# Optimization experiments

Hardware: AMD Instinct MI355X
Metric: run time of the kernel (lower is better)

Reference implementation:

```python
import jax, jax.numpy as jnp
import numpy as np

B, H, O, M = 8192, 1024, 1024, 4

def setup_inputs() -> dict:
    key = jax.random.key(0)
    ks = jax.random.split(key, 8)
    state = jax.random.normal(ks[0], (B, H), dtype=jnp.float32)
    spectral_entropy = jax.random.uniform(ks[1], (B, 1), dtype=jnp.float32)
    curvature = jax.random.normal(ks[2], (B, 1), dtype=jnp.float32)
    # learned params
    modulation_basis = jax.random.normal(ks[3], (M, H, O), dtype=jnp.float32)
    gate_w = jax.random.normal(ks[4], (1, M), dtype=jnp.float32) / jnp.sqrt(1.0)
    gate_b = jax.random.normal(ks[5], (M,), dtype=jnp.float32) * 0.01
    prj_w = jax.random.normal(ks[6], (H, O), dtype=jnp.float32) / jnp.sqrt(H)
    prj_b = jax.random.normal(ks[7], (O,), dtype=jnp.float32) * 0.01
    return {"state": state, "spectral_entropy": spectral_entropy, "curvature": curvature,
            "modulation_basis": modulation_basis, "gate_w": gate_w, "gate_b": gate_b,
            "prj_w": prj_w, "prj_b": prj_b}

def reference(state, spectral_entropy, curvature, modulation_basis, gate_w, gate_b, prj_w, prj_b):
    # softmax gate over modes: [B, M]
    mod_weights = jax.nn.softmax(spectral_entropy @ gate_w + gate_b, axis=-1)
    # Algebraically fused form of einsum('bm,mho->bho') then einsum('bh,bho->bo'):
    # compute per-mode matvec results [B, M, O] (small), then mode-weighted sum.
    mode_out = jnp.einsum('bh,mho->bmo', state, modulation_basis)
    mischief_output = jnp.einsum('bm,bmo->bo', mod_weights, mode_out)
    base_output = state @ prj_w + prj_b
    mix = jax.nn.sigmoid(curvature)  # [B, 1]
    return (1.0 - mix) * base_output + mix * mischief_output
```

## Files before the change

### kernel.cpp

```cpp
#include <hip/hip_runtime.h>
#include <stdint.h>

typedef __attribute__((ext_vector_type(4))) float  float4v;
typedef __attribute__((ext_vector_type(8))) __bf16 bf16x8;
typedef __attribute__((ext_vector_type(8))) unsigned short ushort8;

#define B_DIM 8192
#define H_DIM 1024
#define O_DIM 1024

static __device__ __forceinline__ unsigned short f32_to_bf16(float f) {
  union { float f; unsigned int u; } v; v.f = f;
  unsigned int u = v.u;
  unsigned int r = u + 0x7FFFu + ((u >> 16) & 1u);
  return (unsigned short)(r >> 16);
}

__global__ void prep_inputs(const float* __restrict__ state,
                            const float* __restrict__ basis,
                            const float* __restrict__ prjw,
                            unsigned short* __restrict__ Abf,
                            unsigned short* __restrict__ Wt) {
  __shared__ __align__(16) unsigned short t[64 * 72];
  int bb = blockIdx.x;
  int tid = threadIdx.x;
  if (bb < 1280) {
    int m = bb >> 8, panel = bb & 255;
    int o0 = (panel & 15) * 64, h0 = (panel >> 4) * 64;
    const float* src = (m < 4) ? (basis + (size_t)m * H_DIM * O_DIM) : prjw;
    int r  = tid >> 4;
    int c4 = (tid & 15) * 4;
#pragma unroll
    for (int p = 0; p < 4; ++p) {
      int h = r + p * 16;
      float4v v = *(const float4v*)(src + (size_t)(h0 + h) * O_DIM + o0 + c4);
      t[(c4 + 0) * 72 + h] = f32_to_bf16(v.x);
      t[(c4 + 1) * 72 + h] = f32_to_bf16(v.y);
      t[(c4 + 2) * 72 + h] = f32_to_bf16(v.z);
      t[(c4 + 3) * 72 + h] = f32_to_bf16(v.w);
    }
    __syncthreads();
#pragma unroll
    for (int i = 0; i < 2; ++i) {
      int C = i * 256 + tid;
      int o = C >> 3, cc = C & 7;
      ushort8 val = *(const ushort8*)(t + o * 72 + cc * 8);
      *(ushort8*)(Wt + ((size_t)m * O_DIM + o0 + o) * H_DIM + h0 + cc * 8) = val;
    }
  } else {
    int i = (bb - 1280) * 256 + tid;
    float4v v0 = ((const float4v*)state)[i * 2];
    float4v v1 = ((const float4v*)state)[i * 2 + 1];
    ushort8 o;
    o[0] = f32_to_bf16(v0.x); o[1] = f32_to_bf16(v0.y);
    o[2] = f32_to_bf16(v0.z); o[3] = f32_to_bf16(v0.w);
    o[4] = f32_to_bf16(v1.x); o[5] = f32_to_bf16(v1.y);
    o[6] = f32_to_bf16(v1.z); o[7] = f32_to_bf16(v1.w);
    ((ushort8*)Abf)[i] = o;
  }
}

__global__ __launch_bounds__(256, 2)
void gemm_fused(const unsigned short* __restrict__ A,
                const unsigned short* __restrict__ Wt,
                const float* __restrict__ se, const float* __restrict__ curv,
                const float* __restrict__ gw, const float* __restrict__ gb,
                const float* __restrict__ prjb,
                float* __restrict__ out) {
  __shared__ __align__(16) unsigned char smem[59904];
  float* scf = (float*)(smem + 57344);

  const int tid  = threadIdx.x;
  const int lane = tid & 63;
  const int wave = tid >> 6;
  const int row0 = blockIdx.x * 128;
  const int col0 = blockIdx.y * 64;
  const int wrow = (wave >> 1) * 64;
  const int wcol = (wave & 1) * 32;
  const int q  = lane >> 4;
  const int ln = lane & 15;

  if (tid < 128) {
    int b = row0 + tid;
    float s = se[b];
    float l0 = fmaf(s, gw[0], gb[0]);
    float l1 = fmaf(s, gw[1], gb[1]);
    float l2 = fmaf(s, gw[2], gb[2]);
    float l3 = fmaf(s, gw[3], gb[3]);
    float mx = fmaxf(fmaxf(l0, l1), fmaxf(l2, l3));
    float e0 = __expf(l0 - mx), e1 = __expf(l1 - mx);
    float e2 = __expf(l2 - mx), e3 = __expf(l3 - mx);
    float mix = 1.0f / (1.0f + __expf(-curv[b]));
    float inv = mix / (e0 + e1 + e2 + e3);
    scf[0 * 128 + tid] = e0 * inv;
    scf[1 * 128 + tid] = e1 * inv;
    scf[2 * 128 + tid] = e2 * inv;
    scf[3 * 128 + tid] = e3 * inv;
    scf[4 * 128 + tid] = 1.0f - mix;
  }

  const unsigned short* gA[2];
  unsigned int ldsA[2];
#pragma unroll
  for (int j = 0; j < 2; ++j) {
    int C = (wave * 2 + j) * 64 + lane;
    int row = C >> 2, pos = C & 3;
    int g = pos ^ ((row >> 1) & 3);
    gA[j] = A + (size_t)(row0 + row) * H_DIM + g * 8;
    ldsA[j] = (wave * 2 + j) * 1024;
  }
  const unsigned short* gB[5];
  unsigned int ldsBbase = 8192 + wave * 1024;
  {
    int C = wave * 64 + lane;
    int row = C >> 2, pos = C & 3;
    int g = pos ^ ((row >> 1) & 3);
#pragma unroll
    for (int m = 0; m < 5; ++m)
      gB[m] = Wt + (size_t)m * O_DIM * H_DIM + (size_t)(col0 + row) * H_DIM + g * 8;
  }

  float4v acc[5][4][2];
#pragma unroll
  for (int m = 0; m < 5; ++m)
#pragma unroll
    for (int i = 0; i < 4; ++i)
#pragma unroll
      for (int j = 0; j < 2; ++j)
        acc[m][i][j] = (float4v){0.f, 0.f, 0.f, 0.f};

#define ISSUE_STAGE(s)                                                          \
  do {                                                                          \
    const int _buf = (s) & 1;                                                   \
    const int _k = (s) * 32;                                                    \
    unsigned char* _base = smem + _buf * 28672;                                 \
    _Pragma("unroll")                                                           \
    for (int _j = 0; _j < 2; ++_j)                                              \
      __builtin_amdgcn_global_load_lds(                                         \
          (const __attribute__((address_space(1))) void*)(gA[_j] + _k),         \
          (__attribute__((address_space(3))) void*)(_base + ldsA[_j]), 16, 0, 0);\
    _Pragma("unroll")                                                           \
    for (int _m = 0; _m < 5; ++_m)                                              \
      __builtin_amdgcn_global_load_lds(                                         \
          (const __attribute__((address_space(1))) void*)(gB[_m] + _k),         \
          (__attribute__((address_space(3))) void*)(_base + ldsBbase + _m * 4096),\
          16, 0, 0);                                                            \
  } while (0)

#define COMPUTE_STAGE(s)                                                        \
  do {                                                                          \
    const unsigned short* _sA = (const unsigned short*)(smem + ((s) & 1) * 28672);\
    const unsigned short* _sB = _sA + 4096;                                     \
    bf16x8 _af[4];                                                              \
    _Pragma("unroll")                                                           \
    for (int _t = 0; _t < 4; ++_t) {                                            \
      int _ra = wrow + _t * 16 + ln;                                            \
      int _ps = q ^ ((_ra >> 1) & 3);                                           \
      _af[_t] = *(const bf16x8*)(_sA + _ra * 32 + _ps * 8);                     \
    }                                                                           \
    _Pragma("unroll")                                                           \
    for (int _m = 0; _m < 5; ++_m) {                                            \
      bf16x8 _b0, _b1;                                                          \
      {                                                                         \
        int _rb = wcol + ln;                                                    \
        int _p0 = q ^ ((_rb >> 1) & 3);                                         \
        _b0 = *(const bf16x8*)(_sB + _m * 2048 + _rb * 32 + _p0 * 8);           \
        int _r1 = wcol + 16 + ln;                                               \
        int _p1 = q ^ ((_r1 >> 1) & 3);                                         \
        _b1 = *(const bf16x8*)(_sB + _m * 2048 + _r1 * 32 + _p1 * 8);           \
      }                                                                         \
      _Pragma("unroll")                                                         \
      for (int _ti = 0; _ti < 4; ++_ti) {                                       \
        acc[_m][_ti][0] = __builtin_amdgcn_mfma_f32_16x16x32_bf16(              \
            _af[_ti], _b0, acc[_m][_ti][0], 0, 0, 0);                           \
        acc[_m][_ti][1] = __builtin_amdgcn_mfma_f32_16x16x32_bf16(              \
            _af[_ti], _b1, acc[_m][_ti][1], 0, 0, 0);                           \
      }                                                                         \
    }                                                                           \
  } while (0)

  ISSUE_STAGE(0);
  __syncthreads();
#pragma unroll 2
  for (int s = 0; s < 31; ++s) {
    ISSUE_STAGE(s + 1);
    COMPUTE_STAGE(s);
    __syncthreads();
  }
  COMPUTE_STAGE(31);

  __syncthreads();
  float* fbuf = (float*)smem;
#pragma unroll
  for (int ti = 0; ti < 4; ++ti) {
    int rl = wrow + ti * 16 + q * 4;
#pragma unroll
    for (int tj = 0; tj < 2; ++tj) {
      int cc = wcol + tj * 16 + ln;
#pragma unroll
      for (int r = 0; r < 4; ++r) {
        float v = 0.f;
#pragma unroll
        for (int m = 0; m < 5; ++m)
          v += scf[m * 128 + rl + r] * acc[m][ti][tj][r];
        fbuf[(rl + r) * 68 + cc] = v;
      }
    }
  }
  __syncthreads();
#pragma unroll
  for (int i = 0; i < 8; ++i) {
    int L = i * 256 + tid;
    int row = L >> 4, c4 = L & 15;
    float4v v = *(const float4v*)(fbuf + row * 68 + c4 * 4);
    float cb = scf[4 * 128 + row];
    float4v pb = *(const float4v*)(prjb + col0 + c4 * 4);
    v += cb * pb;
    *(float4v*)(out + (size_t)(row0 + row) * O_DIM + col0 + c4 * 4) = v;
  }
#undef ISSUE_STAGE
#undef COMPUTE_STAGE
}

extern "C" void kernel_launch(void* const* d_in, const int* in_sizes, int n_in,
                              void* d_out, int out_size, void* d_ws, size_t ws_size,
                              hipStream_t stream) {
  const float* state = (const float*)d_in[0];
  const float* se    = (const float*)d_in[1];
  const float* curv  = (const float*)d_in[2];
  const float* basis = (const float*)d_in[3];
  const float* gw    = (const float*)d_in[4];
  const float* gb    = (const float*)d_in[5];
  const float* prjw  = (const float*)d_in[6];
  const float* prjb  = (const float*)d_in[7];
  float* out = (float*)d_out;

  char* ws = (char*)d_ws;
  unsigned short* Abf = (unsigned short*)ws;
  unsigned short* Wt  = (unsigned short*)(ws + (size_t)16 * 1024 * 1024);

  prep_inputs<<<5376, 256, 0, stream>>>(state, basis, prjw, Abf, Wt);
  dim3 gg(B_DIM / 128, O_DIM / 64);
  gemm_fused<<<gg, 256, 0, stream>>>(Abf, Wt, se, curv, gw, gb, prjb, out);
}
```

Before: 183.7 us.

## Fuse state bf16 cast into GEMM and load operands directly from global memory

Drops the separate cast of state to bf16 in the prep kernel; the GEMM now reads fp32 state rows directly and packs them to bf16 in registers. It also removes the LDS double-buffered global_load_lds pipeline and has each wave load its A and B fragments straight from global memory into registers, shrinking shared memory to the epilogue buffer. This avoids a 16 MB bf16 intermediate write/read and the LDS staging barriers. The cost is that every wave re-reads A and B fragments from global or cache with no LDS sharing or software prefetch, and the A traffic doubles because it is fp32.

```diff
diff --git a/kernel.cpp b/kernel.cpp
--- a/kernel.cpp
+++ b/kernel.cpp
@@ -8,6 +8,7 @@
 #define B_DIM 8192
 #define H_DIM 1024
 #define O_DIM 1024
+#define MSTRIDE (O_DIM * H_DIM)
 
 static __device__ __forceinline__ unsigned short f32_to_bf16(float f) {
   union { float f; unsigned int u; } v; v.f = f;
@@ -16,59 +17,54 @@
   return (unsigned short)(r >> 16);
 }
 
-__global__ void prep_inputs(const float* __restrict__ state,
-                            const float* __restrict__ basis,
-                            const float* __restrict__ prjw,
-                            unsigned short* __restrict__ Abf,
-                            unsigned short* __restrict__ Wt) {
+static __device__ __forceinline__ bf16x8 pack8(float4v a, float4v b) {
+  union { ushort8 u; bf16x8 h; } c;
+  c.u[0] = f32_to_bf16(a.x); c.u[1] = f32_to_bf16(a.y);
+  c.u[2] = f32_to_bf16(a.z); c.u[3] = f32_to_bf16(a.w);
+  c.u[4] = f32_to_bf16(b.x); c.u[5] = f32_to_bf16(b.y);
+  c.u[6] = f32_to_bf16(b.z); c.u[7] = f32_to_bf16(b.w);
+  return c.h;
+}
+
+__global__ void transpose_cast(const float* __restrict__ basis, const float* __restrict__ prjw,
+                               unsigned short* __restrict__ Wt) {
   __shared__ __align__(16) unsigned short t[64 * 72];
   int bb = blockIdx.x;
+  int m = bb >> 8, panel = bb & 255;
+  int o0 = (panel & 15) * 64, h0 = (panel >> 4) * 64;
+  const float* src = (m < 4) ? (basis + (size_t)m * H_DIM * O_DIM) : prjw;
   int tid = threadIdx.x;
-  if (bb < 1280) {
-    int m = bb >> 8, panel = bb & 255;
-    int o0 = (panel & 15) * 64, h0 = (panel >> 4) * 64;
-    const float* src = (m < 4) ? (basis + (size_t)m * H_DIM * O_DIM) : prjw;
-    int r  = tid >> 4;
-    int c4 = (tid & 15) * 4;
+  int r  = tid >> 4;
+  int c4 = (tid & 15) * 4;
 #pragma unroll
-    for (int p = 0; p < 4; ++p) {
-      int h = r + p * 16;
-      float4v v = *(const float4v*)(src + (size_t)(h0 + h) * O_DIM + o0 + c4);
-      t[(c4 + 0) * 72 + h] = f32_to_bf16(v.x);
-      t[(c4 + 1) * 72 + h] = f32_to_bf16(v.y);
-      t[(c4 + 2) * 72 + h] = f32_to_bf16(v.z);
-      t[(c4 + 3) * 72 + h] = f32_to_bf16(v.w);
-    }
-    __syncthreads();
+  for (int p = 0; p < 4; ++p) {
+    int h = r + p * 16;
+    float4v v = *(const float4v*)(src + (size_t)(h0 + h) * O_DIM + o0 + c4);
+    t[(c4 + 0) * 72 + h] = f32_to_bf16(v.x);
+    t[(c4 + 1) * 72 + h] = f32_to_bf16(v.y);
+    t[(c4 + 2) * 72 + h] = f32_to_bf16(v.z);
+    t[(c4 + 3) * 72 + h] = f32_to_bf16(v.w);
+  }
+  __syncthreads();
 #pragma unroll
-    for (int i = 0; i < 2; ++i) {
-      int C = i * 256 + tid;
-      int o = C >> 3, cc = C & 7;
-      ushort8 val = *(const ushort8*)(t + o * 72 + cc * 8);
-      *(ushort8*)(Wt + ((size_t)m * O_DIM + o0 + o) * H_DIM + h0 + cc * 8) = val;
-    }
-  } else {
-    int i = (bb - 1280) * 256 + tid;
-    float4v v0 = ((const float4v*)state)[i * 2];
-    float4v v1 = ((const float4v*)state)[i * 2 + 1];
-    ushort8 o;
-    o[0] = f32_to_bf16(v0.x); o[1] = f32_to_bf16(v0.y);
-    o[2] = f32_to_bf16(v0.z); o[3] = f32_to_bf16(v0.w);
-    o[4] = f32_to_bf16(v1.x); o[5] = f32_to_bf16(v1.y);
-    o[6] = f32_to_bf16(v1.z); o[7] = f32_to_bf16(v1.w);
-    ((ushort8*)Abf)[i] = o;
+  for (int i = 0; i < 2; ++i) {
+    int C = i * 256 + tid;
+    int o = C >> 3, cc = C & 7;
+    ushort8 val = *(const ushort8*)(t + o * 72 + cc * 8);
+    *(ushort8*)(Wt + ((size_t)m * O_DIM + o0 + o) * H_DIM + h0 + cc * 8) = val;
   }
 }
 
 __global__ __launch_bounds__(256, 2)
-void gemm_fused(const unsigned short* __restrict__ A,
+void gemm_fused(const float* __restrict__ state,
                 const unsigned short* __restrict__ Wt,
                 const float* __restrict__ se, const float* __restrict__ curv,
                 const float* __restrict__ gw, const float* __restrict__ gb,
                 const float* __restrict__ prjb,
                 float* __restrict__ out) {
-  __shared__ __align__(16) unsigned char smem[59904];
-  float* scf = (float*)(smem + 57344);
+  __shared__ __align__(16) unsigned char smem[37376];
+  float* fbuf = (float*)smem;
+  float* scf  = (float*)(smem + 34816);
 
   const int tid  = threadIdx.x;
   const int lane = tid & 63;
@@ -99,26 +95,12 @@
     scf[4 * 128 + tid] = 1.0f - mix;
   }
 
-  const unsigned short* gA[2];
-  unsigned int ldsA[2];
+  const float* aptr[4];
 #pragma unroll
-  for (int j = 0; j < 2; ++j) {
-    int C = (wave * 2 + j) * 64 + lane;
-    int row = C >> 2, pos = C & 3;
-    int g = pos ^ ((row >> 1) & 3);
-    gA[j] = A + (size_t)(row0 + row) * H_DIM + g * 8;
-    ldsA[j] = (wave * 2 + j) * 1024;
-  }
-  const unsigned short* gB[5];
-  unsigned int ldsBbase = 8192 + wave * 1024;
-  {
-    int C = wave * 64 + lane;
-    int row = C >> 2, pos = C & 3;
-    int g = pos ^ ((row >> 1) & 3);
-#pragma unroll
-    for (int m = 0; m < 5; ++m)
-      gB[m] = Wt + (size_t)m * O_DIM * H_DIM + (size_t)(col0 + row) * H_DIM + g * 8;
-  }
+  for (int t = 0; t < 4; ++t)
+    aptr[t] = state + (size_t)(row0 + wrow + t * 16 + ln) * H_DIM + q * 8;
+  const unsigned short* bptr0 = Wt + (size_t)(col0 + wcol + ln)      * H_DIM + q * 8;
+  const unsigned short* bptr1 = Wt + (size_t)(col0 + wcol + 16 + ln) * H_DIM + q * 8;
 
   float4v acc[5][4][2];
 #pragma unroll
@@ -129,68 +111,29 @@
       for (int j = 0; j < 2; ++j)
         acc[m][i][j] = (float4v){0.f, 0.f, 0.f, 0.f};
 
-#define ISSUE_STAGE(s)                                                          \
-  do {                                                                          \
-    const int _buf = (s) & 1;                                                   \
-    const int _k = (s) * 32;                                                    \
-    unsigned char* _base = smem + _buf * 28672;                                 \
-    _Pragma("unroll")                                                           \
-    for (int _j = 0; _j < 2; ++_j)                                              \
-      __builtin_amdgcn_global_load_lds(                                         \
-          (const __attribute__((address_space(1))) void*)(gA[_j] + _k),         \
-          (__attribute__((address_space(3))) void*)(_base + ldsA[_j]), 16, 0, 0);\
-    _Pragma("unroll")                                                           \
-    for (int _m = 0; _m < 5; ++_m)                                              \
-      __builtin_amdgcn_global_load_lds(                                         \
-          (const __attribute__((address_space(1))) void*)(gB[_m] + _k),         \
-          (__attribute__((address_space(3))) void*)(_base + ldsBbase + _m * 4096),\
-          16, 0, 0);                                                            \
-  } while (0)
-
-#define COMPUTE_STAGE(s)                                                        \
-  do {                                                                          \
-    const unsigned short* _sA = (const unsigned short*)(smem + ((s) & 1) * 28672);\
-    const unsigned short* _sB = _sA + 4096;                                     \
-    bf16x8 _af[4];                                                              \
-    _Pragma("unroll")                                                           \
-    for (int _t = 0; _t < 4; ++_t) {                                            \
-      int _ra = wrow + _t * 16 + ln;                                            \
-      int _ps = q ^ ((_ra >> 1) & 3);                                           \
-      _af[_t] = *(const bf16x8*)(_sA + _ra * 32 + _ps * 8);                     \
-    }                                                                           \
-    _Pragma("unroll")                                                           \
-    for (int _m = 0; _m < 5; ++_m) {                                            \
-      bf16x8 _b0, _b1;                                                          \
-      {                                                                         \
-        int _rb = wcol + ln;                                                    \
-        int _p0 = q ^ ((_rb >> 1) & 3);                                         \
-        _b0 = *(const bf16x8*)(_sB + _m * 2048 + _rb * 32 + _p0 * 8);           \
-        int _r1 = wcol + 16 + ln;                                               \
-        int _p1 = q ^ ((_r1 >> 1) & 3);                                         \
-        _b1 = *(const bf16x8*)(_sB + _m * 2048 + _r1 * 32 + _p1 * 8);           \
-      }                                                                         \
-      _Pragma("unroll")                                                         \
-      for (int _ti = 0; _ti < 4; ++_ti) {                                       \
-        acc[_m][_ti][0] = __builtin_amdgcn_mfma_f32_16x16x32_bf16(              \
-            _af[_ti], _b0, acc[_m][_ti][0], 0, 0, 0);                           \
-        acc[_m][_ti][1] = __builtin_amdgcn_mfma_f32_16x16x32_bf16(              \
-            _af[_ti], _b1, acc[_m][_ti][1], 0, 0, 0);                           \
-      }                                                                         \
-    }                                                                           \
-  } while (0)
-
-  ISSUE_STAGE(0);
-  __syncthreads();
 #pragma unroll 2
-  for (int s = 0; s < 31; ++s) {
-    ISSUE_STAGE(s + 1);
-    COMPUTE_STAGE(s);
-    __syncthreads();
+  for (int s = 0; s < 32; ++s) {
+    const int k = s * 32;
+    bf16x8 af[4];
+#pragma unroll
+    for (int t = 0; t < 4; ++t) {
+      float4v u0 = *(const float4v*)(aptr[t] + k);
+      float4v u1 = *(const float4v*)(aptr[t] + k + 4);
+      af[t] = pack8(u0, u1);
+    }
+#pragma unroll
+    for (int m = 0; m < 5; ++m) {
+      bf16x8 b0 = *(const bf16x8*)(bptr0 + (size_t)m * MSTRIDE + k);
+      bf16x8 b1 = *(const bf16x8*)(bptr1 + (size_t)m * MSTRIDE + k);
+#pragma unroll
+      for (int ti = 0; ti < 4; ++ti) {
+        acc[m][ti][0] = __builtin_amdgcn_mfma_f32_16x16x32_bf16(af[ti], b0, acc[m][ti][0], 0, 0, 0);
+        acc[m][ti][1] = __builtin_amdgcn_mfma_f32_16x16x32_bf16(af[ti], b1, acc[m][ti][1], 0, 0, 0);
+      }
+    }
   }
-  COMPUTE_STAGE(31);
 
   __syncthreads();
-  float* fbuf = (float*)smem;
 #pragma unroll
   for (int ti = 0; ti < 4; ++ti) {
     int rl = wrow + ti * 16 + q * 4;
@@ -218,8 +161,6 @@
     v += cb * pb;
     *(float4v*)(out + (size_t)(row0 + row) * O_DIM + col0 + c4 * 4) = v;
   }
-#undef ISSUE_STAGE
-#undef COMPUTE_STAGE
 }
 
 extern "C" void kernel_launch(void* const* d_in, const int* in_sizes, int n_in,
@@ -235,11 +176,9 @@
   const float* prjb  = (const float*)d_in[7];
   float* out = (float*)d_out;
 
-  char* ws = (char*)d_ws;
-  unsigned short* Abf = (unsigned short*)ws;
-  unsigned short* Wt  = (unsigned short*)(ws + (size_t)16 * 1024 * 1024);
+  unsigned short* Wt = (unsigned short*)d_ws;
 
-  prep_inputs<<<5376, 256, 0, stream>>>(state, basis, prjw, Abf, Wt);
+  transpose_cast<<<1280, 256, 0, stream>>>(basis, prjw, Wt);
   dim3 gg(B_DIM / 128, O_DIM / 64);
-  gemm_fused<<<gg, 256, 0, stream>>>(Abf, Wt, se, curv, gw, gb, prjb, out);
+  gemm_fused<<<gg, 256, 0, stream>>>(state, Wt, se, curv, gw, gb, prjb, out);
 }
```

New measurement: 378.9 us. 106% more time.

## Apply per-row mode coefficients each k-step to shrink accumulators to one set

Applied to the files above, without the earlier changes.

Instead of keeping five separate MFMA accumulator sets (one per mode plus base) and combining them with per-row coefficients at the end, each MFMA now starts from zero and its result is scaled by per-row coefficients held in registers and added into a single accumulator set. This cuts accumulator registers roughly fivefold, which could raise occupancy or stop spills. In exchange it adds a vector FMA per MFMA, so the accumulation chain runs through VALU ops and MFMA outputs cannot be chained, which may stall the matrix pipe. Rounding also shifts slightly because the scaling happens per k-step.

```diff
diff --git a/kernel.cpp b/kernel.cpp
--- a/kernel.cpp
+++ b/kernel.cpp
@@ -120,20 +120,10 @@
       gB[m] = Wt + (size_t)m * O_DIM * H_DIM + (size_t)(col0 + row) * H_DIM + g * 8;
   }
 
-  float4v acc[5][4][2];
-#pragma unroll
-  for (int m = 0; m < 5; ++m)
-#pragma unroll
-    for (int i = 0; i < 4; ++i)
-#pragma unroll
-      for (int j = 0; j < 2; ++j)
-        acc[m][i][j] = (float4v){0.f, 0.f, 0.f, 0.f};
-
 #define ISSUE_STAGE(s)                                                          \
   do {                                                                          \
-    const int _buf = (s) & 1;                                                   \
+    unsigned char* _base = smem + ((s) & 1) * 28672;                            \
     const int _k = (s) * 32;                                                    \
-    unsigned char* _base = smem + _buf * 28672;                                 \
     _Pragma("unroll")                                                           \
     for (int _j = 0; _j < 2; ++_j)                                              \
       __builtin_amdgcn_global_load_lds(                                         \
@@ -147,49 +137,59 @@
           16, 0, 0);                                                            \
   } while (0)
 
-#define COMPUTE_STAGE(s)                                                        \
-  do {                                                                          \
-    const unsigned short* _sA = (const unsigned short*)(smem + ((s) & 1) * 28672);\
-    const unsigned short* _sB = _sA + 4096;                                     \
-    bf16x8 _af[4];                                                              \
-    _Pragma("unroll")                                                           \
-    for (int _t = 0; _t < 4; ++_t) {                                            \
-      int _ra = wrow + _t * 16 + ln;                                            \
-      int _ps = q ^ ((_ra >> 1) & 3);                                           \
-      _af[_t] = *(const bf16x8*)(_sA + _ra * 32 + _ps * 8);                     \
-    }                                                                           \
-    _Pragma("unroll")                                                           \
-    for (int _m = 0; _m < 5; ++_m) {                                            \
-      bf16x8 _b0, _b1;                                                          \
-      {                                                                         \
-        int _rb = wcol + ln;                                                    \
-        int _p0 = q ^ ((_rb >> 1) & 3);                                         \
-        _b0 = *(const bf16x8*)(_sB + _m * 2048 + _rb * 32 + _p0 * 8);           \
-        int _r1 = wcol + 16 + ln;                                               \
-        int _p1 = q ^ ((_r1 >> 1) & 3);                                         \
-        _b1 = *(const bf16x8*)(_sB + _m * 2048 + _r1 * 32 + _p1 * 8);           \
-      }                                                                         \
-      _Pragma("unroll")                                                         \
-      for (int _ti = 0; _ti < 4; ++_ti) {                                       \
-        acc[_m][_ti][0] = __builtin_amdgcn_mfma_f32_16x16x32_bf16(              \
-            _af[_ti], _b0, acc[_m][_ti][0], 0, 0, 0);                           \
-        acc[_m][_ti][1] = __builtin_amdgcn_mfma_f32_16x16x32_bf16(              \
-            _af[_ti], _b1, acc[_m][_ti][1], 0, 0, 0);                           \
-      }                                                                         \
-    }                                                                           \
-  } while (0)
+  float4v oacc[4][2];
+#pragma unroll
+  for (int i = 0; i < 4; ++i)
+#pragma unroll
+    for (int j = 0; j < 2; ++j)
+      oacc[i][j] = (float4v){0.f, 0.f, 0.f, 0.f};
 
   ISSUE_STAGE(0);
   __syncthreads();
+
+  float4v creg[5][4];
+#pragma unroll
+  for (int m = 0; m < 5; ++m)
+#pragma unroll
+    for (int ti = 0; ti < 4; ++ti)
+      creg[m][ti] = *(const float4v*)(scf + m * 128 + wrow + ti * 16 + q * 4);
+
+  const float4v zf = (float4v){0.f, 0.f, 0.f, 0.f};
+
 #pragma unroll 2
-  for (int s = 0; s < 31; ++s) {
-    ISSUE_STAGE(s + 1);
-    COMPUTE_STAGE(s);
+  for (int s = 0; s < 32; ++s) {
+    if (s < 31) ISSUE_STAGE(s + 1);
+    {
+      const unsigned short* sAb = (const unsigned short*)(smem + (s & 1) * 28672);
+      const unsigned short* sBb = sAb + 4096;
+      bf16x8 af[4];
+#pragma unroll
+      for (int t = 0; t < 4; ++t) {
+        int ra = wrow + t * 16 + ln;
+        int ps = q ^ ((ra >> 1) & 3);
+        af[t] = *(const bf16x8*)(sAb + ra * 32 + ps * 8);
+      }
+#pragma unroll
+      for (int m = 0; m < 5; ++m) {
+        int rb0 = wcol + ln;
+        int p0  = q ^ ((rb0 >> 1) & 3);
+        bf16x8 b0 = *(const bf16x8*)(sBb + m * 2048 + rb0 * 32 + p0 * 8);
+        int rb1 = wcol + 16 + ln;
+        int p1  = q ^ ((rb1 >> 1) & 3);
+        bf16x8 b1 = *(const bf16x8*)(sBb + m * 2048 + rb1 * 32 + p1 * 8);
+#pragma unroll
+        for (int ti = 0; ti < 4; ++ti) {
+          float4v t0 = __builtin_amdgcn_mfma_f32_16x16x32_bf16(af[ti], b0, zf, 0, 0, 0);
+          oacc[ti][0] += creg[m][ti] * t0;
+          float4v t1 = __builtin_amdgcn_mfma_f32_16x16x32_bf16(af[ti], b1, zf, 0, 0, 0);
+          oacc[ti][1] += creg[m][ti] * t1;
+        }
+      }
+    }
     __syncthreads();
   }
-  COMPUTE_STAGE(31);
-
-  __syncthreads();
+#undef ISSUE_STAGE
+
   float* fbuf = (float*)smem;
 #pragma unroll
   for (int ti = 0; ti < 4; ++ti) {
@@ -198,13 +198,8 @@
     for (int tj = 0; tj < 2; ++tj) {
       int cc = wcol + tj * 16 + ln;
 #pragma unroll
-      for (int r = 0; r < 4; ++r) {
-        float v = 0.f;
-#pragma unroll
-        for (int m = 0; m < 5; ++m)
-          v += scf[m * 128 + rl + r] * acc[m][ti][tj][r];
-        fbuf[(rl + r) * 68 + cc] = v;
-      }
+      for (int r = 0; r < 4; ++r)
+        fbuf[(rl + r) * 68 + cc] = oacc[ti][tj][r];
     }
   }
   __syncthreads();
@@ -218,8 +213,6 @@
     v += cb * pb;
     *(float4v*)(out + (size_t)(row0 + row) * O_DIM + col0 + c4 * 4) = v;
   }
-#undef ISSUE_STAGE
-#undef COMPUTE_STAGE
 }
 
 extern "C" void kernel_launch(void* const* d_in, const int* in_sizes, int n_in,
```

Result: slower. 205.6 us (+11.9%).
